# Kernel tuning notes

Measured on AMD Instinct MI355X. Metric: run time of the kernel, lower is better.

Reference implementation:

```python
import jax, jax.numpy as jnp
import numpy as np

B, T, D = 64, 256, 300
H = 256            # each_state = state_size // 2
G = 4 * H          # gate dim = state_size * 2
N = 8              # num_bases
M, KQ = 64, 64     # meta_dim, key_query_size
V = 10000          # meta vocab


def setup_inputs() -> dict:
    key = jax.random.key(0)
    ks = jax.random.split(key, 16)
    s = 0.05
    return {
        'x': jax.random.normal(ks[0], (B, T, D), jnp.float32),
        'length': jax.random.randint(ks[1], (B,), 1, T + 1),
        'user_idx': jax.random.randint(ks[2], (B,), 0, V),
        'item_idx': jax.random.randint(ks[3], (B,), 0, V),
        'user_emb': jax.random.normal(ks[4], (V, M), jnp.float32) * s,
        'item_emb': jax.random.normal(ks[5], (V, M), jnp.float32) * s,
        'W1': jax.random.normal(ks[6], (2 * M, KQ), jnp.float32) * s,
        'b1': jax.random.normal(ks[7], (KQ,), jnp.float32) * s,
        'W2': jax.random.normal(ks[8], (KQ, N), jnp.float32) * s,
        'Wih': jax.random.normal(ks[9], (N, G, D), jnp.float32) * s,
        'Whh': jax.random.normal(ks[10], (N, G, H), jnp.float32) * s,
        'bias': jax.random.normal(ks[11], (N, G), jnp.float32) * s,
        'Wih_r': jax.random.normal(ks[12], (N, G, D), jnp.float32) * s,
        'Whh_r': jax.random.normal(ks[13], (N, G, H), jnp.float32) * s,
        'bias_r': jax.random.normal(ks[14], (N, G), jnp.float32) * s,
    }


def _run_dir(xs, mask, Wi, Wh, bb):
    # xs: [T,B,D], mask: [T,B] True where state forced to zero
    b, h = xs.shape[1], Wh.shape[2]
    h0 = jnp.zeros((b, h), xs.dtype)

    def step(carry, inp):
        hx, cx = carry
        xt, m = inp
        gates = (jnp.einsum('bgi,bi->bg', Wi, xt)
                 + jnp.einsum('bgh,bh->bg', Wh, hx) + bb)
        ig, fg, gg, og = jnp.split(gates, 4, axis=1)
        cy = jax.nn.sigmoid(fg) * cx + jax.nn.sigmoid(ig) * jnp.tanh(gg)
        hy = jax.nn.sigmoid(og) * jnp.tanh(cy)
        cy = jnp.where(m[:, None], 0.0, cy)
        hy = jnp.where(m[:, None], 0.0, hy)
        return (hy, cy), hy

    _, hs = jax.lax.scan(step, (h0, h0), (xs, mask))
    return hs  # [T,B,H]


def reference(x, length, user_idx, item_idx, user_emb, item_emb,
              W1, b1, W2, Wih, Whh, bias, Wih_r, Whh_r, bias_r):
    # basis mixing coefficients per sample
    q = jnp.concatenate([user_emb[user_idx], item_emb[item_idx]], axis=1)  # [B,2M]
    c = jax.nn.softmax(jnp.tanh(q @ W1 + b1) @ W2, axis=1)                 # [B,N]
    mix = lambda w: jnp.einsum('bn,n...->b...', c, w)

    Bc, Tc = x.shape[0], x.shape[1]
    t = jnp.arange(Tc)
    mask_f = t[:, None] >= length[None, :]            # length - 1 < i
    mask_r = (Tc - t)[:, None] > length[None, :]      # maxlength - i > length

    xs = jnp.swapaxes(x, 0, 1)                        # [T,B,D]
    h_f = _run_dir(xs, mask_f, mix(Wih), mix(Whh), mix(bias))
    h_r = _run_dir(xs[::-1], mask_r, mix(Wih_r), mix(Whh_r), mix(bias_r))
    h_r = h_r[::-1]                                   # un-reverse in time
    return jnp.concatenate([h_f, h_r], axis=-1).swapaxes(0, 1)  # [B,T,2H]
```

## Files before the change

kernel.cpp:

```cpp
#include <hip/hip_runtime.h>

#define B_ 64
#define T_ 256
#define D_ 300
#define DP_ 320
#define H_ 256
#define G_ 1024
#define N_ 8

typedef unsigned int u32;
typedef unsigned short u16;
typedef __attribute__((ext_vector_type(8))) short short8;
typedef __attribute__((ext_vector_type(4))) float f32x4;
typedef __attribute__((ext_vector_type(4))) u32 u32x4;
typedef __attribute__((ext_vector_type(2))) u32 u32x2;
typedef _Float16 h2 __attribute__((ext_vector_type(2)));
typedef __fp16 fp16x2 __attribute__((ext_vector_type(2)));

__device__ __forceinline__ u16 f2bf(float f){
  union {float f; u32 u;} v; v.f = f;
  u32 r = (v.u + 0x7fffu + ((v.u>>16)&1u)) >> 16;
  return (u16)r;
}
__device__ __forceinline__ float bflo(u32 u){
  union {u32 u; float f;} v; v.u = u<<16; return v.f;
}
__device__ __forceinline__ float bfhi(u32 u){
  union {u32 u; float f;} v; v.u = u & 0xffff0000u; return v.f;
}
__device__ __forceinline__ float rcp_(float x){
#if __has_builtin(__builtin_amdgcn_rcpf)
  return __builtin_amdgcn_rcpf(x);
#else
  return 1.0f/x;
#endif
}
__device__ __forceinline__ float sigm(float x){ return rcp_(1.0f + __expf(-x)); }
__device__ __forceinline__ float tanh_(float x){ return fmaf(2.0f, rcp_(1.0f + __expf(-2.0f*x)), -1.0f); }

__device__ __forceinline__ float fdot2(u32 a, u32 b, float c){
  union { u32 u; h2 h; } ua, ub; ua.u = a; ub.u = b;
#if __has_builtin(__builtin_amdgcn_fdot2)
  return __builtin_amdgcn_fdot2(ua.h, ub.h, c, false);
#else
  return c + (float)ua.h.x*(float)ub.h.x + (float)ua.h.y*(float)ub.h.y;
#endif
}
__device__ __forceinline__ u32 pkf16(float a, float b){
  union { fp16x2 h; u32 u; } v; v.h = __builtin_amdgcn_cvt_pkrtz(a, b); return v.u;
}
__device__ __forceinline__ float qred(float v){
  union {float f; int i;} u, t;
  u.f = v;
  t.i = __builtin_amdgcn_mov_dpp(u.i, 0xB1, 0xF, 0xF, true);
  u.f += t.f;
  t.i = __builtin_amdgcn_mov_dpp(u.i, 0x4E, 0xF, 0xF, true);
  return u.f + t.f;
}

__global__ void __launch_bounds__(64) k_coef(
    const int* __restrict__ uidx, const int* __restrict__ iidx,
    const float* __restrict__ uemb, const float* __restrict__ iemb,
    const float* __restrict__ W1, const float* __restrict__ b1,
    const float* __restrict__ W2, float* __restrict__ coef)
{
  __shared__ float q[128];
  __shared__ float hid[64];
  __shared__ float lg[8];
  int b = blockIdx.x, t = threadIdx.x;
  int u = uidx[b], it = iidx[b];
  q[t]      = uemb[(size_t)u*64 + t];
  q[64 + t] = iemb[(size_t)it*64 + t];
  __syncthreads();
  float s = b1[t];
  for (int j = 0; j < 128; ++j) s = fmaf(q[j], W1[j*64 + t], s);
  hid[t] = tanhf(s);
  __syncthreads();
  if (t < 8) {
    float s2 = 0.f;
    for (int j = 0; j < 64; ++j) s2 = fmaf(hid[j], W2[j*8 + t], s2);
    lg[t] = s2;
  }
  __syncthreads();
  if (t == 0) {
    float mx = lg[0];
    for (int n = 1; n < 8; ++n) mx = fmaxf(mx, lg[n]);
    float e[8], den = 0.f;
    for (int n = 0; n < 8; ++n){ e[n] = __expf(lg[n]-mx); den += e[n]; }
    for (int n = 0; n < 8; ++n) coef[b*8+n] = e[n]/den;
  }
}

__global__ void __launch_bounds__(256) k_mix_whh(
    const float* __restrict__ Whh_f, const float* __restrict__ Whh_r,
    const float* __restrict__ bias_f, const float* __restrict__ bias_r,
    const float* __restrict__ coef, u32* __restrict__ blob, float* __restrict__ bias_m)
{
  int gblk = blockIdx.x;
  int dir  = blockIdx.y;
  int b0   = blockIdx.z * 32;
  int tid  = threadIdx.x;
  const float* Wsel = dir ? Whh_r : Whh_f;
  const float* bsel = dir ? bias_r : bias_f;
  __shared__ float bs[N_][8][H_];
  for (int v = 0; v < 64; ++v){
    int i = v*256 + tid;
    int n = i >> 11, gl = (i >> 8) & 7, c = i & 255;
    bs[n][gl][c] = Wsel[((size_t)n*G_ + gblk*8 + gl)*H_ + c];
  }
  __syncthreads();
  int t2l = tid & 7, ii = tid >> 3;
  int tid2 = gblk*8 + t2l;
  int gg = tid2 >> 2, q = tid2 & 3;
  int cidx = ii >> 2, e = ii & 3;
  int p = q*32 + ((cidx + 2*q)&7)*4 + e;
  int glbase = gg*4 - gblk*8;
  float bw0[4][8], bw1[4][8];
  #pragma unroll
  for (int l = 0; l < 4; ++l)
    #pragma unroll
    for (int n = 0; n < 8; ++n){
      bw0[l][n] = bs[n][glbase + l][2*p];
      bw1[l][n] = bs[n][glbase + l][2*p + 1];
    }
  for (int bb_ = 0; bb_ < 32; ++bb_){
    int b = b0 + bb_;
    float c8[8];
    #pragma unroll
    for (int n = 0; n < 8; ++n) c8[n] = coef[b*8+n];
    u32x4 ov;
    #pragma unroll
    for (int l = 0; l < 4; ++l){
      float w0 = 0.f, w1 = 0.f;
      #pragma unroll
      for (int n = 0; n < 8; ++n){ w0 = fmaf(c8[n], bw0[l][n], w0); w1 = fmaf(c8[n], bw1[l][n], w1); }
      ov[l] = pkf16(w0, w1);
    }
    size_t chain = (size_t)(dir*B_ + b);
    *(u32x4*)(blob + ((chain*32 + ii)*1024 + tid2)*4) = ov;
    if (tid < 8){
      float bv = 0.f;
      #pragma unroll
      for (int n = 0; n < 8; ++n) bv = fmaf(c8[n], bsel[n*G_ + gblk*8 + tid], bv);
      bias_m[chain*G_ + gblk*8 + tid] = bv;
    }
  }
}

__global__ void __launch_bounds__(256) k_mix_wi(
    const float* __restrict__ Wih_f, const float* __restrict__ Wih_r,
    const float* __restrict__ coef, u32* __restrict__ WimU)
{
  int gblk = blockIdx.x;
  int dir  = blockIdx.y;
  int b0   = blockIdx.z * 32;
  int tid  = threadIdx.x;
  const float* Wsel = dir ? Wih_r : Wih_f;
  __shared__ float bs[N_][8][D_];
  for (int v = 0; v < 75; ++v){
    int i = v*256 + tid;
    int n = i/2400, rem = i%2400, gl = rem/300, c = rem%300;
    bs[n][gl][c] = Wsel[((size_t)n*G_ + gblk*8 + gl)*D_ + c];
  }
  __syncthreads();
  float bw[5][2][8];
  int rowv[5], cpv[5];
  #pragma unroll
  for (int v = 0; v < 5; ++v){
    int idx = v*256 + tid;
    int row = idx/160, cp = idx%160;
    rowv[v] = row; cpv[v] = cp;
    #pragma unroll
    for (int n = 0; n < 8; ++n){
      bw[v][0][n] = (cp < 150) ? bs[n][row][2*cp]   : 0.f;
      bw[v][1][n] = (cp < 150) ? bs[n][row][2*cp+1] : 0.f;
    }
  }
  for (int bb_ = 0; bb_ < 32; ++bb_){
    int b = b0 + bb_;
    float c8[8];
    #pragma unroll
    for (int n = 0; n < 8; ++n) c8[n] = coef[b*8+n];
    #pragma unroll
    for (int v = 0; v < 5; ++v){
      float w0 = 0.f, w1 = 0.f;
      #pragma unroll
      for (int n = 0; n < 8; ++n){ w0 = fmaf(c8[n], bw[v][0][n], w0); w1 = fmaf(c8[n], bw[v][1][n], w1); }
      WimU[(((size_t)(dir*B_+b)*G_ + gblk*8 + rowv[v])*160) + cpv[v]] = (u32)f2bf(w0) | ((u32)f2bf(w1) << 16);
    }
  }
}

__global__ void __launch_bounds__(256) k_xpad(const float* __restrict__ x, u32* __restrict__ xpadU)
{
  int o = blockIdx.x*256 + threadIdx.x;
  int bt = o/160, cp = o%160;
  float v0 = (cp < 150) ? x[(size_t)bt*D_ + 2*cp]   : 0.f;
  float v1 = (cp < 150) ? x[(size_t)bt*D_ + 2*cp+1] : 0.f;
  xpadU[o] = (u32)f2bf(v0) | ((u32)f2bf(v1) << 16);
}

__global__ void __launch_bounds__(256,2) k_gemm(
    const u16* __restrict__ xpad, const u16* __restrict__ Wim,
    const float* __restrict__ bias_m, u16* __restrict__ xproj)
{
  int bx = blockIdx.x;
  int b  = blockIdx.y, dir = blockIdx.z;
  int tt = bx >> 3, tg = bx & 7;
  int tid = threadIdx.x;
  int wid = tid >> 6, lane = tid & 63;
  int wr = wid >> 1, wc = wid & 1;
  __shared__ u16 As[128][72];
  __shared__ u16 Bs[128][72];
  const u16* Ap = xpad + ((size_t)b*T_ + tt*128)*DP_;
  const u16* Bp = Wim + (((size_t)dir*B_ + b)*G_ + tg*128)*DP_;
  f32x4 acc[4][4];
  #pragma unroll
  for (int i = 0; i < 4; ++i)
    #pragma unroll
    for (int j = 0; j < 4; ++j) acc[i][j] = (f32x4){0.f,0.f,0.f,0.f};
  for (int kt = 0; kt < 5; ++kt){
    int k0 = kt*64;
    #pragma unroll
    for (int i = 0; i < 4; ++i){
      int ci = i*256 + tid;
      int row = ci >> 3, cc = (ci & 7)*8;
      *(u32x4*)&As[row][cc] = *(const u32x4*)(Ap + (size_t)row*DP_ + k0 + cc);
      *(u32x4*)&Bs[row][cc] = *(const u32x4*)(Bp + (size_t)row*DP_ + k0 + cc);
    }
    __syncthreads();
    #pragma unroll
    for (int kk = 0; kk < 2; ++kk){
      short8 af[4], bfr[4];
      #pragma unroll
      for (int mi = 0; mi < 4; ++mi) af[mi]  = *(const short8*)&As[wr*64 + mi*16 + (lane&15)][kk*32 + (lane>>4)*8];
      #pragma unroll
      for (int ni = 0; ni < 4; ++ni) bfr[ni] = *(const short8*)&Bs[wc*64 + ni*16 + (lane&15)][kk*32 + (lane>>4)*8];
      #pragma unroll
      for (int mi = 0; mi < 4; ++mi)
        #pragma unroll
        for (int ni = 0; ni < 4; ++ni)
          acc[mi][ni] = __builtin_amdgcn_mfma_f32_16x16x32_bf16(af[mi], bfr[ni], acc[mi][ni], 0,0,0);
    }
    __syncthreads();
  }
  int r4 = (lane >> 4)*4, cg = lane & 15;
  const float* bmp = bias_m + (size_t)(dir*B_ + b)*G_;
  #pragma unroll
  for (int ni = 0; ni < 4; ++ni){
    int g = tg*128 + wc*64 + ni*16 + cg;
    float bsv = bmp[g];
    #pragma unroll
    for (int mi = 0; mi < 4; ++mi)
      #pragma unroll
      for (int j = 0; j < 4; ++j){
        int t = tt*128 + wr*64 + mi*16 + r4 + j;
        xproj[(((size_t)dir*B_ + b)*T_ + t)*G_ + g] = f2bf(acc[mi][ni][j] + bsv);
      }
  }
}

__global__ void __launch_bounds__(1024) k_rec(
    const u32* __restrict__ blob, const u32* __restrict__ xprojU,
    const int* __restrict__ length, float* __restrict__ out)
{
  int chain = blockIdx.x;
  int dir = chain >> 6, b = chain & 63;
  int tid = threadIdx.x;
  int gg = tid >> 2, q = tid & 3;
  __shared__ u32 wlds[8][1024][4];
  __shared__ __align__(16) float gates4[256][4];
  __shared__ __align__(16) u16 hp16[256];
  const u32* hp32 = (const u32*)hp16;

  u32 w[96];
  const u32* bp = blob + (size_t)chain*32*1024*4;
  #pragma unroll
  for (int ii = 0; ii < 24; ++ii){
    u32x4 v = *(const u32x4*)(bp + ((size_t)ii*1024 + tid)*4);
    w[4*ii] = v.x; w[4*ii+1] = v.y; w[4*ii+2] = v.z; w[4*ii+3] = v.w;
  }
  #pragma unroll
  for (int ii = 24; ii < 32; ++ii){
    u32x4 v = *(const u32x4*)(bp + ((size_t)ii*1024 + tid)*4);
    *(u32x4*)&wlds[ii-24][tid][0] = v;
  }
  if (tid < 256) hp16[tid] = 0;
  int len = length[b];
  const u32* xp = xprojU + (size_t)chain*T_*512;
  float* outp = out + (size_t)b*T_*512 + dir*H_;
  float cst = 0.f;
  __syncthreads();

  for (int step = 0; step < len; ++step){
    int t = dir ? (len-1-step) : step;
    u32 xv0 = 0, xv1 = 0;
    if (q == 0){
      u32x2 xv = *(const u32x2*)(xp + (size_t)t*512 + 2*gg);
      xv0 = xv.x; xv1 = xv.y;
    }
    float a0 = 0.f, a1 = 0.f, a2 = 0.f, a3 = 0.f;
    #pragma unroll
    for (int cidx = 0; cidx < 8; ++cidx){
      int c4 = (cidx + 2*q) & 7;
      u32x4 hq = *(const u32x4*)&hp32[q*32 + c4*4];
      if (cidx < 6){
        #pragma unroll
        for (int e = 0; e < 4; ++e){
          u32 hv = hq[e];
          a0 = fdot2(w[cidx*16 + e*4 + 0], hv, a0);
          a1 = fdot2(w[cidx*16 + e*4 + 1], hv, a1);
          a2 = fdot2(w[cidx*16 + e*4 + 2], hv, a2);
          a3 = fdot2(w[cidx*16 + e*4 + 3], hv, a3);
        }
      } else {
        #pragma unroll
        for (int e = 0; e < 4; ++e){
          u32x4 wv = *(const u32x4*)&wlds[cidx*4 + e - 24][tid][0];
          u32 hv = hq[e];
          a0 = fdot2(wv.x, hv, a0);
          a1 = fdot2(wv.y, hv, a1);
          a2 = fdot2(wv.z, hv, a2);
          a3 = fdot2(wv.w, hv, a3);
        }
      }
    }
    a0 = qred(a0); a1 = qred(a1); a2 = qred(a2); a3 = qred(a3);
    if (q == 0){
      a0 += bflo(xv0); a1 += bfhi(xv0); a2 += bflo(xv1); a3 += bfhi(xv1);
      f32x4 g4; g4.x = a0; g4.y = a1; g4.z = a2; g4.w = a3;
      *(f32x4*)&gates4[gg][0] = g4;
    }
    __syncthreads();
    if (tid < 256){
      const float* gf = &gates4[0][0];
      float ig = gf[tid],       fg = gf[256 + tid];
      float g_ = gf[512 + tid], og = gf[768 + tid];
      float i_ = sigm(ig), f_ = sigm(fg), gt = tanh_(g_), o_ = sigm(og);
      float cn = fmaf(f_, cst, i_*gt);
      float hy = o_ * tanh_(cn);
      cst = cn;
      ((u16*)hp16)[tid] = (u16)(pkf16(hy, hy) & 0xffffu);
      outp[(size_t)t*512 + tid] = hy;
    }
    __syncthreads();
  }
}

extern "C" void kernel_launch(void* const* d_in, const int* in_sizes, int n_in,
                              void* d_out, int out_size, void* d_ws, size_t ws_size,
                              hipStream_t stream)
{
  const float* x      = (const float*)d_in[0];
  const int*   length = (const int*)d_in[1];
  const int*   uidx   = (const int*)d_in[2];
  const int*   iidx   = (const int*)d_in[3];
  const float* uemb   = (const float*)d_in[4];
  const float* iemb   = (const float*)d_in[5];
  const float* W1     = (const float*)d_in[6];
  const float* b1     = (const float*)d_in[7];
  const float* W2     = (const float*)d_in[8];
  const float* Wih    = (const float*)d_in[9];
  const float* Whh    = (const float*)d_in[10];
  const float* bias   = (const float*)d_in[11];
  const float* Wih_r  = (const float*)d_in[12];
  const float* Whh_r  = (const float*)d_in[13];
  const float* bias_r = (const float*)d_in[14];
  float* out = (float*)d_out;
  char* ws = (char*)d_ws;

  float* coef   = (float*)(ws + 0);
  float* bias_m = (float*)(ws + 2048);
  u32*   blob   = (u32*)  (ws + 526336);
  u16*   Wim    = (u16*)  (ws + 67635200);
  u16*   xpad   = (u16*)  (ws + 151521280);
  u16*   xproj  = (u16*)  (ws + 162007040);

  (void)hipMemsetAsync(d_out, 0, (size_t)out_size*sizeof(float), stream);
  if (ws_size < 229115904ull) return;

  hipLaunchKernelGGL(k_coef,    dim3(64),       dim3(64),   0, stream, uidx, iidx, uemb, iemb, W1, b1, W2, coef);
  hipLaunchKernelGGL(k_mix_whh, dim3(128,2,2),  dim3(256),  0, stream, Whh, Whh_r, bias, bias_r, coef, blob, bias_m);
  hipLaunchKernelGGL(k_mix_wi,  dim3(128,2,2),  dim3(256),  0, stream, Wih, Wih_r, coef, (u32*)Wim);
  hipLaunchKernelGGL(k_xpad,    dim3(10240),    dim3(256),  0, stream, x, (u32*)xpad);
  hipLaunchKernelGGL(k_gemm,    dim3(16,64,2),  dim3(256),  0, stream, xpad, Wim, bias_m, xproj);
  hipLaunchKernelGGL(k_rec,     dim3(128),      dim3(1024), 0, stream, blob, (const u32*)xproj, length, out);
}
```

Before: 572.7 us.

## Repartition recurrent matvec to 8 gates per thread with 8-lane DPP reduction

The recurrent step's work split changes. Each thread now computes 8 gate outputs over one eighth of the hidden dimension, instead of 4 gates over one quarter, and the weight-mixing kernel writes the blob in the matching layout. This halves the per-step LDS reads of the hidden state and the number of rotated h-vector loads per thread. In exchange there are more live accumulators and a three-stage DPP reduction (adding a row_half_mirror step) applied to 8 values instead of 4. Only one lane in eight now loads the input projection and writes gates.

```diff
diff --git a/kernel.cpp b/kernel.cpp
--- a/kernel.cpp
+++ b/kernel.cpp
@@ -49,12 +49,14 @@
 __device__ __forceinline__ u32 pkf16(float a, float b){
   union { fp16x2 h; u32 u; } v; v.h = __builtin_amdgcn_cvt_pkrtz(a, b); return v.u;
 }
-__device__ __forceinline__ float qred(float v){
+__device__ __forceinline__ float qred8(float v){
   union {float f; int i;} u, t;
   u.f = v;
   t.i = __builtin_amdgcn_mov_dpp(u.i, 0xB1, 0xF, 0xF, true);
   u.f += t.f;
   t.i = __builtin_amdgcn_mov_dpp(u.i, 0x4E, 0xF, 0xF, true);
+  u.f += t.f;
+  t.i = __builtin_amdgcn_mov_dpp(u.i, 0x141, 0xF, 0xF, true);
   return u.f + t.f;
 }
 
@@ -111,18 +113,20 @@
   __syncthreads();
   int t2l = tid & 7, ii = tid >> 3;
   int tid2 = gblk*8 + t2l;
-  int gg = tid2 >> 2, q = tid2 & 3;
-  int cidx = ii >> 2, e = ii & 3;
-  int p = q*32 + ((cidx + 2*q)&7)*4 + e;
-  int glbase = gg*4 - gblk*8;
+  int r = t2l;
+  int pe = ii >> 1, gh = ii & 1;
+  int cx = pe >> 2, e = pe & 3;
+  int p = r*16 + ((cx + r)&3)*4 + e;
   float bw0[4][8], bw1[4][8];
   #pragma unroll
-  for (int l = 0; l < 4; ++l)
+  for (int l4 = 0; l4 < 4; ++l4){
+    int gl = gh*4 + l4;
     #pragma unroll
     for (int n = 0; n < 8; ++n){
-      bw0[l][n] = bs[n][glbase + l][2*p];
-      bw1[l][n] = bs[n][glbase + l][2*p + 1];
-    }
+      bw0[l4][n] = bs[n][gl][2*p];
+      bw1[l4][n] = bs[n][gl][2*p + 1];
+    }
+  }
   for (int bb_ = 0; bb_ < 32; ++bb_){
     int b = b0 + bb_;
     float c8[8];
@@ -130,11 +134,11 @@
     for (int n = 0; n < 8; ++n) c8[n] = coef[b*8+n];
     u32x4 ov;
     #pragma unroll
-    for (int l = 0; l < 4; ++l){
+    for (int l4 = 0; l4 < 4; ++l4){
       float w0 = 0.f, w1 = 0.f;
       #pragma unroll
-      for (int n = 0; n < 8; ++n){ w0 = fmaf(c8[n], bw0[l][n], w0); w1 = fmaf(c8[n], bw1[l][n], w1); }
-      ov[l] = pkf16(w0, w1);
+      for (int n = 0; n < 8; ++n){ w0 = fmaf(c8[n], bw0[l4][n], w0); w1 = fmaf(c8[n], bw1[l4][n], w1); }
+      ov[l4] = pkf16(w0, w1);
     }
     size_t chain = (size_t)(dir*B_ + b);
     *(u32x4*)(blob + ((chain*32 + ii)*1024 + tid2)*4) = ov;
@@ -267,9 +271,9 @@
   int chain = blockIdx.x;
   int dir = chain >> 6, b = chain & 63;
   int tid = threadIdx.x;
-  int gg = tid >> 2, q = tid & 3;
+  int gset = tid >> 3, r = tid & 7;
   __shared__ u32 wlds[8][1024][4];
-  __shared__ __align__(16) float gates4[256][4];
+  __shared__ __align__(16) float gates8[1024];
   __shared__ __align__(16) u16 hp16[256];
   const u32* hp32 = (const u32*)hp16;
 
@@ -294,46 +298,59 @@
 
   for (int step = 0; step < len; ++step){
     int t = dir ? (len-1-step) : step;
-    u32 xv0 = 0, xv1 = 0;
-    if (q == 0){
-      u32x2 xv = *(const u32x2*)(xp + (size_t)t*512 + 2*gg);
-      xv0 = xv.x; xv1 = xv.y;
-    }
-    float a0 = 0.f, a1 = 0.f, a2 = 0.f, a3 = 0.f;
-    #pragma unroll
-    for (int cidx = 0; cidx < 8; ++cidx){
-      int c4 = (cidx + 2*q) & 7;
-      u32x4 hq = *(const u32x4*)&hp32[q*32 + c4*4];
-      if (cidx < 6){
+    u32x4 xv = (u32x4){0,0,0,0};
+    if (r == 0)
+      xv = *(const u32x4*)(xp + (size_t)t*512 + gset*4);
+    float a0=0.f,a1=0.f,a2=0.f,a3=0.f,a4=0.f,a5=0.f,a6=0.f,a7=0.f;
+    #pragma unroll
+    for (int cx = 0; cx < 4; ++cx){
+      int c4 = (cx + r) & 3;
+      u32x4 hq = *(const u32x4*)&hp32[r*16 + c4*4];
+      if (cx < 3){
         #pragma unroll
         for (int e = 0; e < 4; ++e){
+          int pe = cx*4 + e;
           u32 hv = hq[e];
-          a0 = fdot2(w[cidx*16 + e*4 + 0], hv, a0);
-          a1 = fdot2(w[cidx*16 + e*4 + 1], hv, a1);
-          a2 = fdot2(w[cidx*16 + e*4 + 2], hv, a2);
-          a3 = fdot2(w[cidx*16 + e*4 + 3], hv, a3);
+          a0 = fdot2(w[(pe*2+0)*4 + 0], hv, a0);
+          a1 = fdot2(w[(pe*2+0)*4 + 1], hv, a1);
+          a2 = fdot2(w[(pe*2+0)*4 + 2], hv, a2);
+          a3 = fdot2(w[(pe*2+0)*4 + 3], hv, a3);
+          a4 = fdot2(w[(pe*2+1)*4 + 0], hv, a4);
+          a5 = fdot2(w[(pe*2+1)*4 + 1], hv, a5);
+          a6 = fdot2(w[(pe*2+1)*4 + 2], hv, a6);
+          a7 = fdot2(w[(pe*2+1)*4 + 3], hv, a7);
         }
       } else {
         #pragma unroll
         for (int e = 0; e < 4; ++e){
-          u32x4 wv = *(const u32x4*)&wlds[cidx*4 + e - 24][tid][0];
+          int pe = cx*4 + e;
           u32 hv = hq[e];
-          a0 = fdot2(wv.x, hv, a0);
-          a1 = fdot2(wv.y, hv, a1);
-          a2 = fdot2(wv.z, hv, a2);
-          a3 = fdot2(wv.w, hv, a3);
+          u32x4 wv0 = *(const u32x4*)&wlds[pe*2+0-24][tid][0];
+          u32x4 wv1 = *(const u32x4*)&wlds[pe*2+1-24][tid][0];
+          a0 = fdot2(wv0.x, hv, a0);
+          a1 = fdot2(wv0.y, hv, a1);
+          a2 = fdot2(wv0.z, hv, a2);
+          a3 = fdot2(wv0.w, hv, a3);
+          a4 = fdot2(wv1.x, hv, a4);
+          a5 = fdot2(wv1.y, hv, a5);
+          a6 = fdot2(wv1.z, hv, a6);
+          a7 = fdot2(wv1.w, hv, a7);
         }
       }
     }
-    a0 = qred(a0); a1 = qred(a1); a2 = qred(a2); a3 = qred(a3);
-    if (q == 0){
-      a0 += bflo(xv0); a1 += bfhi(xv0); a2 += bflo(xv1); a3 += bfhi(xv1);
-      f32x4 g4; g4.x = a0; g4.y = a1; g4.z = a2; g4.w = a3;
-      *(f32x4*)&gates4[gg][0] = g4;
+    a0 = qred8(a0); a1 = qred8(a1); a2 = qred8(a2); a3 = qred8(a3);
+    a4 = qred8(a4); a5 = qred8(a5); a6 = qred8(a6); a7 = qred8(a7);
+    if (r == 0){
+      a0 += bflo(xv.x); a1 += bfhi(xv.x); a2 += bflo(xv.y); a3 += bfhi(xv.y);
+      a4 += bflo(xv.z); a5 += bfhi(xv.z); a6 += bflo(xv.w); a7 += bfhi(xv.w);
+      f32x4 g4a; g4a.x=a0; g4a.y=a1; g4a.z=a2; g4a.w=a3;
+      f32x4 g4b; g4b.x=a4; g4b.y=a5; g4b.z=a6; g4b.w=a7;
+      *(f32x4*)&gates8[gset*8 + 0] = g4a;
+      *(f32x4*)&gates8[gset*8 + 4] = g4b;
     }
     __syncthreads();
     if (tid < 256){
-      const float* gf = &gates4[0][0];
+      const float* gf = &gates8[0];
       float ig = gf[tid],       fg = gf[256 + tid];
       float g_ = gf[512 + tid], og = gf[768 + tid];
       float i_ = sigm(ig), f_ = sigm(fg), gt = tanh_(g_), o_ = sigm(og);
```

Result: slower. 625.4 us (+9.2%).
